# Performance work log

Measured on AMD Instinct MI355X. Metric: run time of the kernel, lower is better.

The kernel has to match this reference:

```python
import jax, jax.numpy as jnp
import numpy as np

D_MODEL = 1024
H = 16
D_K = D_MODEL // H
B, S = 4, 2048


def setup_inputs() -> dict:
    key = jax.random.key(0)
    ks = jax.random.split(key, 12)
    s = 1.0 / np.sqrt(D_MODEL)
    inp = {
        "q": jax.random.normal(ks[0], (B, S, D_MODEL), jnp.float32),
        "k": jax.random.normal(ks[1], (B, S, D_MODEL), jnp.float32),
        "v": jax.random.normal(ks[2], (B, S, D_MODEL), jnp.float32),
        "mask": jax.random.randint(ks[3], (1, 1, S, S), 0, 2, jnp.int32),
        # torch nn.Linear convention: weight [out, in], y = x @ W.T + b
        "w_q": jax.random.uniform(ks[4], (D_MODEL, D_MODEL), jnp.float32, -s, s),
        "b_q": jax.random.uniform(ks[5], (D_MODEL,), jnp.float32, -s, s),
        "w_k": jax.random.uniform(ks[6], (D_MODEL, D_MODEL), jnp.float32, -s, s),
        "b_k": jax.random.uniform(ks[7], (D_MODEL,), jnp.float32, -s, s),
        "w_v": jax.random.uniform(ks[8], (D_MODEL, D_MODEL), jnp.float32, -s, s),
        "b_v": jax.random.uniform(ks[9], (D_MODEL,), jnp.float32, -s, s),
        "w_o": jax.random.uniform(ks[10], (D_MODEL, D_MODEL), jnp.float32, -s, s),
        "b_o": jax.random.uniform(ks[11], (D_MODEL,), jnp.float32, -s, s),
    }
    return inp


def _split_heads(x):
    b, s, _ = x.shape
    return x.reshape(b, s, H, D_K).transpose(0, 2, 1, 3)  # [B,H,S,Dk]


def reference(q, k, v, mask, w_q, b_q, w_k, b_k, w_v, b_v, w_o, b_o):
    query = _split_heads(q @ w_q.T + b_q)
    key = _split_heads(k @ w_k.T + b_k)
    value = _split_heads(v @ w_v.T + b_v)
    scores = jnp.einsum("bhqd,bhkd->bhqk", query, key) / jnp.sqrt(
        jnp.asarray(D_K, query.dtype))
    scores = jnp.where(mask == 0, jnp.asarray(-1e9, scores.dtype), scores)
    attn = jax.nn.softmax(scores, axis=-1)  # dropout p=0 (eval) -> identity
    x = jnp.einsum("bhqk,bhkd->bhqd", attn, value)
    x = x.transpose(0, 2, 1, 3).reshape(q.shape[0], -1, H * D_K)
    return x @ w_o.T + b_o
```

## Files before the change

### kernel.cpp

```cpp
#include <hip/hip_runtime.h>

typedef __bf16 bf16_t;
typedef __bf16 bf16x4 __attribute__((ext_vector_type(4)));
typedef __bf16 bf16x8 __attribute__((ext_vector_type(8)));
typedef float f32x4 __attribute__((ext_vector_type(4)));
typedef float f32x16 __attribute__((ext_vector_type(16)));
typedef unsigned int uint;
typedef uint uint2v __attribute__((ext_vector_type(2)));
typedef uint uint4v __attribute__((ext_vector_type(4)));

#define CSCALE 0.18033688011112042f

static __device__ __forceinline__ bf16_t f2bf(float f) {
  unsigned u = __builtin_bit_cast(unsigned, f);
  u = (u + 0x7fff + ((u >> 16) & 1)) >> 16;
  unsigned short h = (unsigned short)u;
  return __builtin_bit_cast(bf16_t, h);
}
static __device__ __forceinline__ uint cvt_pk(float a, float b) {
  uint r;
  asm("v_cvt_pk_bf16_f32 %0, %1, %2" : "=v"(r) : "v"(a), "v"(b));
  return r;
}

#define GLD_LDS(g, l) \
  __builtin_amdgcn_global_load_lds((const __attribute__((address_space(1))) void*)(g), \
                                   (__attribute__((address_space(3))) void*)(l), 16, 0, 0)
#define VMCNT(n) asm volatile("s_waitcnt vmcnt(" #n ")" ::: "memory")
#define LGKM0() asm volatile("s_waitcnt lgkmcnt(0)" ::: "memory")
#define BARRIER() do { __builtin_amdgcn_s_barrier(); __builtin_amdgcn_sched_barrier(0); } while (0)

__global__ void cvt4_f2b(const float* __restrict__ a, const float* __restrict__ b,
                         const float* __restrict__ c, const float* __restrict__ d,
                         bf16_t* __restrict__ oa, bf16_t* __restrict__ ob,
                         bf16_t* __restrict__ oc, bf16_t* __restrict__ od) {
  int i = blockIdx.x * 256 + threadIdx.x;
  const float* src = a;
  bf16_t* dst = oa;
  int w = i >> 18;
  i &= 262143;
  if (w == 1) { src = b; dst = ob; }
  else if (w == 2) { src = c; dst = oc; }
  else if (w == 3) { src = d; dst = od; }
  const float4 f = reinterpret_cast<const float4*>(src)[i];
  bf16x4 o;
  o[0] = f2bf(f.x); o[1] = f2bf(f.y); o[2] = f2bf(f.z); o[3] = f2bf(f.w);
  reinterpret_cast<bf16x4*>(dst)[i] = o;
}

__global__ void mask_bits_k(const int* __restrict__ m, uint* __restrict__ out) {
  int i = blockIdx.x * 256 + threadIdx.x;
  int q = i & 2047, t = i >> 11;
  const int* mrow = m + (size_t)q * 2048 + t * 32;
  uint bits = 0;
#pragma unroll
  for (int j = 0; j < 16; ++j) {
    int r0 = (j & 3) + 8 * (j >> 2);
    bits |= (mrow[r0] ? 1u : 0u) << j;
    bits |= (mrow[r0 + 4] ? 1u : 0u) << (16 + j);
  }
  out[(size_t)t * 2048 + q] = bits;
}

__global__ __launch_bounds__(256, 2) void qkv_gemm(
    const float* __restrict__ qA, const float* __restrict__ kA, const float* __restrict__ vA,
    const bf16_t* __restrict__ wq, const bf16_t* __restrict__ wk, const bf16_t* __restrict__ wv,
    const float* __restrict__ bq, const float* __restrict__ bk, const float* __restrict__ bv,
    bf16_t* __restrict__ Qp, bf16_t* __restrict__ Kp, bf16_t* __restrict__ Vt) {
  constexpr int K = 1024;
  __shared__ __align__(16) bf16_t AsB[2][128 * 32];
  __shared__ __align__(16) bf16_t BsB[3][256 * 32];
  const int z = blockIdx.z;
  const float* A = (z == 0) ? qA : (z == 1) ? kA : vA;
  const bf16_t* W = (z == 0) ? wq : (z == 1) ? wk : wv;
  const float* bias = (z == 0) ? bq : (z == 1) ? bk : bv;

  const int tid = threadIdx.x;
  const int lane = tid & 63;
  const int wv_ = tid >> 6;
  const int wm = (wv_ & 1) * 64, wn = (wv_ >> 1) * 128;
  const int l15 = lane & 15, lhi = lane >> 4;
  const int bm = blockIdx.x, bn = blockIdx.y;

  const int arow0 = tid >> 3;
  const int acol = tid & 7;
  const float* gA = A + (size_t)(bm * 128 + arow0) * K + acol * 4;
  const int brows = tid >> 2;
  const bf16_t* gB = W + (size_t)(bn * 256 + brows) * K + ((tid & 3) ^ (brows & 3)) * 8;

  f32x4 acc[4][8] = {};
  f32x4 rA0[4], rA1[4];

  auto A_LOAD = [&](int t, f32x4* R) {
#pragma unroll
    for (int L = 0; L < 4; ++L)
      R[L] = *reinterpret_cast<const f32x4*>(gA + (size_t)L * 32 * K + t * 32);
  };
  auto A_WRITE = [&](const f32x4* R, int buf) {
#pragma unroll
    for (int L = 0; L < 4; ++L) {
      int row = arow0 + L * 32;
      uint2v u;
      u[0] = cvt_pk(R[L][0], R[L][1]);
      u[1] = cvt_pk(R[L][2], R[L][3]);
      char* p = (char*)&AsB[buf][0] + row * 64 + (((acol >> 1) ^ (row & 3)) * 16) + (acol & 1) * 8;
      *reinterpret_cast<uint2v*>(p) = u;
    }
  };
  auto B_STAGE = [&](int t, int buf) {
#pragma unroll
    for (int c2 = 0; c2 < 4; ++c2)
      GLD_LDS(gB + (size_t)c2 * 64 * K + t * 32, (char*)&BsB[buf][0] + c2 * 4096 + wv_ * 1024);
  };
  auto COMPUTE = [&](int ba, int bb) {
    bf16x8 af[4], bfv[8];
#pragma unroll
    for (int i = 0; i < 4; ++i) {
      int arow = wm + i * 16 + l15;
      af[i] = *reinterpret_cast<const bf16x8*>(
          (const char*)&AsB[ba][0] + arow * 64 + ((lhi ^ (arow & 3)) * 16));
    }
#pragma unroll
    for (int j = 0; j < 8; ++j) {
      int br = wn + j * 16 + l15;
      bfv[j] = *reinterpret_cast<const bf16x8*>(
          (const char*)&BsB[bb][0] + br * 64 + ((lhi ^ (br & 3)) * 16));
    }
#pragma unroll
    for (int i = 0; i < 4; ++i)
#pragma unroll
      for (int j = 0; j < 8; ++j)
        acc[i][j] = __builtin_amdgcn_mfma_f32_16x16x32_bf16(af[i], bfv[j], acc[i][j], 0, 0, 0);
  };

#define QSTEP(T, RL, RW, BAW, BAC, BBC, BBS) \
  A_LOAD((T) + 2, RL); B_STAGE((T) + 2, BBS); \
  COMPUTE(BAC, BBC); \
  VMCNT(8); \
  A_WRITE(RW, BAW); \
  LGKM0(); BARRIER();

  A_LOAD(0, rA0); B_STAGE(0, 0);
  A_LOAD(1, rA1); B_STAGE(1, 1);
  VMCNT(8);
  A_WRITE(rA0, 0);
  LGKM0(); BARRIER();

#pragma unroll 1
  for (int t6 = 0; t6 < 30; t6 += 6) {
    QSTEP(t6 + 0, rA0, rA1, 1, 0, 0, 2)
    QSTEP(t6 + 1, rA1, rA0, 0, 1, 1, 0)
    QSTEP(t6 + 2, rA0, rA1, 1, 0, 2, 1)
    QSTEP(t6 + 3, rA1, rA0, 0, 1, 0, 2)
    QSTEP(t6 + 4, rA0, rA1, 1, 0, 1, 0)
    QSTEP(t6 + 5, rA1, rA0, 0, 1, 2, 1)
  }
  COMPUTE(0, 0);
  VMCNT(4);
  A_WRITE(rA1, 1);
  VMCNT(0);
  LGKM0(); BARRIER();
  COMPUTE(1, 1);

  if (z == 2) {
    const int b = (bm * 128) >> 11;
    const int s0 = (bm * 128) & 2047;
    bf16_t* vb = Vt + ((size_t)b * 1024 + bn * 256 + wn + l15) * 2048 + s0 + wm + lhi * 4;
#pragma unroll
    for (int j = 0; j < 8; ++j) {
      float bv2 = bias[bn * 256 + wn + j * 16 + l15];
#pragma unroll
      for (int i = 0; i < 4; ++i) {
        bf16x4 pk;
#pragma unroll
        for (int r = 0; r < 4; ++r) pk[r] = f2bf(acc[i][j][r] + bv2);
        *reinterpret_cast<bf16x4*>(vb + (size_t)(j * 16) * 2048 + i * 16) = pk;
      }
    }
  } else {
    bf16_t* O = (z == 0) ? Qp : Kp;
    const float scale = (z == 0) ? CSCALE : 1.0f;
#pragma unroll
    for (int i = 0; i < 4; ++i) {
#pragma unroll
      for (int j = 0; j < 8; ++j) {
        int n = bn * 256 + wn + j * 16 + l15;
        float bv2 = bias[n];
#pragma unroll
        for (int r = 0; r < 4; ++r) {
          int m = bm * 128 + wm + i * 16 + lhi * 4 + r;
          O[(size_t)m * 1024 + n] = f2bf((acc[i][j][r] + bv2) * scale);
        }
      }
    }
  }
#undef QSTEP
}

__global__ __launch_bounds__(256, 2) void gemm_o(
    const bf16_t* __restrict__ A, const bf16_t* __restrict__ Bw,
    const float* __restrict__ bias, float* __restrict__ Cout) {
  constexpr int K = 1024;
  __shared__ __align__(16) bf16_t As[3][128 * 32];
  __shared__ __align__(16) bf16_t Bs[3][256 * 32];
  const int tid = threadIdx.x;
  const int lane = tid & 63;
  const int wv_ = tid >> 6;
  const int wm = (wv_ & 1) * 64, wn = (wv_ >> 1) * 128;
  const int l15 = lane & 15, lhi = lane >> 4;
  const int bm = blockIdx.x, bn = blockIdx.y;
  const int rws = tid >> 2;
  const bf16_t* ga = A + (size_t)(bm * 128 + rws) * K + ((tid & 3) ^ (rws & 3)) * 8;
  const bf16_t* gb = Bw + (size_t)(bn * 256 + rws) * K + ((tid & 3) ^ (rws & 3)) * 8;
  f32x4 acc[4][8] = {};

  auto STAGE = [&](int t, int buf) {
#pragma unroll
    for (int c2 = 0; c2 < 2; ++c2)
      GLD_LDS(ga + (size_t)c2 * 64 * K + t * 32, (char*)&As[buf][0] + c2 * 4096 + wv_ * 1024);
#pragma unroll
    for (int c2 = 0; c2 < 4; ++c2)
      GLD_LDS(gb + (size_t)c2 * 64 * K + t * 32, (char*)&Bs[buf][0] + c2 * 4096 + wv_ * 1024);
  };
  auto COMPUTE = [&](int buf) {
    bf16x8 af[4], bfv[8];
#pragma unroll
    for (int i = 0; i < 4; ++i) {
      int arow = wm + i * 16 + l15;
      af[i] = *reinterpret_cast<const bf16x8*>(
          (const char*)&As[buf][0] + arow * 64 + ((lhi ^ (arow & 3)) * 16));
    }
#pragma unroll
    for (int j = 0; j < 8; ++j) {
      int br = wn + j * 16 + l15;
      bfv[j] = *reinterpret_cast<const bf16x8*>(
          (const char*)&Bs[buf][0] + br * 64 + ((lhi ^ (br & 3)) * 16));
    }
#pragma unroll
    for (int i = 0; i < 4; ++i)
#pragma unroll
      for (int j = 0; j < 8; ++j)
        acc[i][j] = __builtin_amdgcn_mfma_f32_16x16x32_bf16(af[i], bfv[j], acc[i][j], 0, 0, 0);
  };

  STAGE(0, 0);
  STAGE(1, 1);
#pragma unroll 1
  for (int tt = 0; tt < 30; tt += 3) {
    VMCNT(6); BARRIER(); COMPUTE(0); STAGE(tt + 2, 2);
    VMCNT(6); BARRIER(); COMPUTE(1); STAGE(tt + 3, 0);
    VMCNT(6); BARRIER(); COMPUTE(2); STAGE(tt + 4, 1);
  }
  VMCNT(6); BARRIER(); COMPUTE(0);
  VMCNT(0); BARRIER(); COMPUTE(1);

#pragma unroll
  for (int i = 0; i < 4; ++i)
#pragma unroll
    for (int j = 0; j < 8; ++j) {
      int n = bn * 256 + wn + j * 16 + l15;
      float bv2 = bias[n];
#pragma unroll
      for (int r = 0; r < 4; ++r) {
        int m = bm * 128 + wm + i * 16 + lhi * 4 + r;
        Cout[(size_t)m * 1024 + n] = acc[i][j][r] + bv2;
      }
    }
}

static __device__ __forceinline__ void qk2(const bf16_t* Kbuf, const bf16x8 qfA[4],
                                           const bf16x8 qfB[4], int l31, int h,
                                           f32x16& sA, f32x16& sB) {
  sA = {}; sB = {};
  __builtin_amdgcn_s_setprio(1);
#pragma unroll
  for (int c = 0; c < 4; ++c) {
    bf16x8 kf = *reinterpret_cast<const bf16x8*>(Kbuf + l31 * 72 + h * 8 + 16 * c);
    sA = __builtin_amdgcn_mfma_f32_32x32x16_bf16(kf, qfA[c], sA, 0, 0, 0);
    sB = __builtin_amdgcn_mfma_f32_32x32x16_bf16(kf, qfB[c], sB, 0, 0, 0);
  }
  __builtin_amdgcn_s_setprio(0);
}

static __device__ __forceinline__ void softmax_tile(
    const f32x16& sv, uint mb, int h, f32x16& o0, f32x16& o1,
    float& mrun, float& lsum, bf16x8& pa0, bf16x8& pa1) {
  const uint mbh = mb >> (h << 4);
  float a0 = fmaxf(fmaxf(sv[0], sv[1]), sv[2]);
  float a1 = fmaxf(fmaxf(sv[3], sv[4]), sv[5]);
  float a2 = fmaxf(fmaxf(sv[6], sv[7]), sv[8]);
  float a3 = fmaxf(fmaxf(sv[9], sv[10]), sv[11]);
  float a4 = fmaxf(fmaxf(sv[12], sv[13]), sv[14]);
  float b0 = fmaxf(fmaxf(a0, a1), a2);
  float mt = fmaxf(fmaxf(b0, fmaxf(a3, a4)), sv[15]);
  if (!__all(mt - mrun <= 8.0f)) {
    float mtf = fmaxf(mt, __shfl_xor(mt, 32));
    float mnew = fmaxf(mrun, mtf);
    float alpha = __builtin_amdgcn_exp2f(mrun - mnew);
    lsum *= alpha;
#pragma unroll
    for (int r = 0; r < 16; ++r) {
      float ar = __shfl(alpha, (r & 3) + 8 * (r >> 2) + 4 * h);
      o0[r] *= ar; o1[r] *= ar;
    }
    mrun = mnew;
  }
  float p[16];
#pragma unroll
  for (int r = 0; r < 16; ++r) {
    float pv = __builtin_amdgcn_exp2f(sv[r] - mrun);
    uint smask = (uint)__builtin_amdgcn_sbfe((int)mbh, r, 1);
    p[r] = __builtin_bit_cast(float, __builtin_bit_cast(uint, pv) & smask);
  }
  float t0 = p[0] + p[1], t1 = p[2] + p[3], t2 = p[4] + p[5], t3 = p[6] + p[7];
  float t4 = p[8] + p[9], t5 = p[10] + p[11], t6 = p[12] + p[13], t7 = p[14] + p[15];
  t0 += t1; t2 += t3; t4 += t5; t6 += t7;
  lsum += (t0 + t2) + (t4 + t6);
  uint dw[8];
#pragma unroll
  for (int i = 0; i < 8; ++i) dw[i] = cvt_pk(p[2 * i], p[2 * i + 1]);
  uint e0 = (uint)__shfl_xor((int)(h ? dw[0] : dw[2]), 32);
  uint e1 = (uint)__shfl_xor((int)(h ? dw[1] : dw[3]), 32);
  uint e2 = (uint)__shfl_xor((int)(h ? dw[4] : dw[6]), 32);
  uint e3 = (uint)__shfl_xor((int)(h ? dw[5] : dw[7]), 32);
  uint4v ua0 = {h ? e0 : dw[0], h ? e1 : dw[1], h ? dw[2] : e0, h ? dw[3] : e1};
  uint4v ua1 = {h ? e2 : dw[4], h ? e3 : dw[5], h ? dw[6] : e2, h ? dw[7] : e3};
  pa0 = __builtin_bit_cast(bf16x8, ua0);
  pa1 = __builtin_bit_cast(bf16x8, ua1);
}

static __device__ __forceinline__ void pv2(const bf16_t* Vbuf,
                                           bf16x8 paA0, bf16x8 paA1, bf16x8 paB0, bf16x8 paB1,
                                           int l31, int h,
                                           f32x16& oA0, f32x16& oA1, f32x16& oB0, f32x16& oB1) {
  bf16x8 v00 = *reinterpret_cast<const bf16x8*>(Vbuf + l31 * 40 + h * 8);
  bf16x8 v01 = *reinterpret_cast<const bf16x8*>(Vbuf + l31 * 40 + 16 + h * 8);
  bf16x8 v10 = *reinterpret_cast<const bf16x8*>(Vbuf + (32 + l31) * 40 + h * 8);
  bf16x8 v11 = *reinterpret_cast<const bf16x8*>(Vbuf + (32 + l31) * 40 + 16 + h * 8);
  __builtin_amdgcn_s_setprio(1);
  oA0 = __builtin_amdgcn_mfma_f32_32x32x16_bf16(paA0, v00, oA0, 0, 0, 0);
  oA0 = __builtin_amdgcn_mfma_f32_32x32x16_bf16(paA1, v01, oA0, 0, 0, 0);
  oA1 = __builtin_amdgcn_mfma_f32_32x32x16_bf16(paA0, v10, oA1, 0, 0, 0);
  oA1 = __builtin_amdgcn_mfma_f32_32x32x16_bf16(paA1, v11, oA1, 0, 0, 0);
  oB0 = __builtin_amdgcn_mfma_f32_32x32x16_bf16(paB0, v00, oB0, 0, 0, 0);
  oB0 = __builtin_amdgcn_mfma_f32_32x32x16_bf16(paB1, v01, oB0, 0, 0, 0);
  oB1 = __builtin_amdgcn_mfma_f32_32x32x16_bf16(paB0, v10, oB1, 0, 0, 0);
  oB1 = __builtin_amdgcn_mfma_f32_32x32x16_bf16(paB1, v11, oB1, 0, 0, 0);
  __builtin_amdgcn_s_setprio(0);
}

__global__ __launch_bounds__(256, 2) void attn_kernel(
    const bf16_t* __restrict__ Qp, const bf16_t* __restrict__ Kp,
    const bf16_t* __restrict__ Vt, const uint* __restrict__ maskbits,
    bf16_t* __restrict__ Xb) {
  constexpr int S = 2048, D = 1024;
  __shared__ __align__(16) bf16_t Ks[2][32][72];
  __shared__ __align__(16) bf16_t Vs[2][64][40];
  const int tid = threadIdx.x;
  const int wv_ = tid >> 6, lane = tid & 63;
  const int l31 = lane & 31, h = lane >> 5;
  const int blk = blockIdx.x;
  const int bh = blk & 63, qt = blk >> 6;
  const int b = bh >> 4, hd = bh & 15;
  const int q0 = qt * 256 + wv_ * 64;

  const int rK = tid >> 3, sK = tid & 7;
  const int rV = tid >> 2, sV = tid & 3;
  const bf16_t* gK = Kp + ((size_t)b * S + rK) * D + hd * 64 + sK * 8;
  const bf16_t* gV = Vt + ((size_t)b * 1024 + hd * 64 + rV) * (size_t)S + sV * 8;
  bf16_t* wK0 = &Ks[0][rK][sK * 8];
  bf16_t* wK1 = &Ks[1][rK][sK * 8];
  bf16_t* wV0 = &Vs[0][rV][sV * 8];
  bf16_t* wV1 = &Vs[1][rV][sV * 8];

  const bf16_t* qbase = Qp + (size_t)(b * S + q0 + l31) * D + hd * 64 + h * 8;
  bf16x8 qfA[4], qfB[4];
#pragma unroll
  for (int c = 0; c < 4; ++c) {
    qfA[c] = *reinterpret_cast<const bf16x8*>(qbase + 16 * c);
    qfB[c] = *reinterpret_cast<const bf16x8*>(qbase + (size_t)32 * D + 16 * c);
  }

  const uint* mbase = maskbits + q0 + l31;

  f32x16 oA0 = {}, oA1 = {}, oB0 = {}, oB1 = {};
  float mrunA = 0.f, lsumA = 0.f, mrunB = 0.f, lsumB = 0.f;
  bf16x8 paA0, paA1, paB0, paB1;

  {
    bf16x8 k0 = *reinterpret_cast<const bf16x8*>(gK);
    bf16x8 k1 = *reinterpret_cast<const bf16x8*>(gK + (size_t)32 * D);
    bf16x8 v0 = *reinterpret_cast<const bf16x8*>(gV);
    *reinterpret_cast<bf16x8*>(wK0) = k0;
    *reinterpret_cast<bf16x8*>(wK1) = k1;
    *reinterpret_cast<bf16x8*>(wV0) = v0;
  }
  uint mbA = mbase[0], mbB = mbase[32];
  __syncthreads();
  {
    f32x16 sA, sB;
    qk2(&Ks[0][0][0], qfA, qfB, l31, h, sA, sB);
    softmax_tile(sA, mbA, h, oA0, oA1, mrunA, lsumA, paA0, paA1);
    softmax_tile(sB, mbB, h, oB0, oB1, mrunB, lsumB, paB0, paB1);
  }

  auto body = [&](int j, bf16_t* wK_st, bf16_t* wV_st, const bf16_t* Kq,
                  const bf16_t* Vp, bool stageK) {
    bf16x8 kreg, vreg;
    if (stageK) kreg = *reinterpret_cast<const bf16x8*>(gK + (size_t)(j + 2) * 32 * D);
    vreg = *reinterpret_cast<const bf16x8*>(gV + (size_t)(j + 1) * 32);
    uint mnA = mbase[(size_t)(j + 1) * 2048];
    uint mnB = mbase[(size_t)(j + 1) * 2048 + 32];
    f32x16 sA, sB;
    qk2(Kq, qfA, qfB, l31, h, sA, sB);
    pv2(Vp, paA0, paA1, paB0, paB1, l31, h, oA0, oA1, oB0, oB1);
    softmax_tile(sA, mnA, h, oA0, oA1, mrunA, lsumA, paA0, paA1);
    softmax_tile(sB, mnB, h, oB0, oB1, mrunB, lsumB, paB0, paB1);
    if (stageK) *reinterpret_cast<bf16x8*>(wK_st) = kreg;
    *reinterpret_cast<bf16x8*>(wV_st) = vreg;
    __syncthreads();
  };

#pragma unroll 1
  for (int jj = 0; jj < 31; ++jj) {
    const int j = 2 * jj;
    body(j,     wK0, wV1, &Ks[1][0][0], &Vs[0][0][0], true);
    body(j + 1, wK1, wV0, &Ks[0][0][0], &Vs[1][0][0], true);
  }
  body(62, wK0, wV1, &Ks[1][0][0], &Vs[0][0][0], false);
  pv2(&Vs[1][0][0], paA0, paA1, paB0, paB1, l31, h, oA0, oA1, oB0, oB1);

  lsumA += __shfl_xor(lsumA, 32);
  lsumB += __shfl_xor(lsumB, 32);
  float linvA = __builtin_amdgcn_rcpf(lsumA);
  float linvB = __builtin_amdgcn_rcpf(lsumB);
  bf16_t* xrow = Xb + (size_t)(b * S + q0) * D + hd * 64 + l31;
#pragma unroll
  for (int r = 0; r < 16; ++r) {
    int qrow = (r & 3) + 8 * (r >> 2) + 4 * h;
    float lrA = __shfl(linvA, qrow);
    float lrB = __shfl(linvB, qrow);
    xrow[(size_t)qrow * D] = f2bf(oA0[r] * lrA);
    xrow[(size_t)qrow * D + 32] = f2bf(oA1[r] * lrA);
    xrow[(size_t)(qrow + 32) * D] = f2bf(oB0[r] * lrB);
    xrow[(size_t)(qrow + 32) * D + 32] = f2bf(oB1[r] * lrB);
  }
}

extern "C" void kernel_launch(void* const* d_in, const int* in_sizes, int n_in,
                              void* d_out, int out_size, void* d_ws, size_t ws_size,
                              hipStream_t stream) {
  const float* q = (const float*)d_in[0];
  const float* k = (const float*)d_in[1];
  const float* v = (const float*)d_in[2];
  const int* mask = (const int*)d_in[3];
  const float* w_q = (const float*)d_in[4];
  const float* b_q = (const float*)d_in[5];
  const float* w_k = (const float*)d_in[6];
  const float* b_k = (const float*)d_in[7];
  const float* w_v = (const float*)d_in[8];
  const float* b_v = (const float*)d_in[9];
  const float* w_o = (const float*)d_in[10];
  const float* b_o = (const float*)d_in[11];

  char* ws = (char*)d_ws;
  const size_t SZ = (size_t)8192 * 1024 * 2;
  bf16_t* Qp = (bf16_t*)(ws + 0 * SZ);
  bf16_t* Kp = (bf16_t*)(ws + 1 * SZ);
  bf16_t* Vt = (bf16_t*)(ws + 2 * SZ);
  bf16_t* Xb = (bf16_t*)(ws + 3 * SZ);
  uint* maskB = (uint*)(ws + 4 * SZ);
  bf16_t* wqb = (bf16_t*)(ws + 4 * SZ + 8388608);
  bf16_t* wkb = wqb + 1048576;
  bf16_t* wvb = wkb + 1048576;
  bf16_t* wob = wvb + 1048576;

  cvt4_f2b<<<4096, 256, 0, stream>>>(w_q, w_k, w_v, w_o, wqb, wkb, wvb, wob);
  mask_bits_k<<<512, 256, 0, stream>>>(mask, maskB);

  dim3 g3(64, 4, 3);
  qkv_gemm<<<g3, 256, 0, stream>>>(q, k, v, wqb, wkb, wvb, b_q, b_k, b_v, Qp, Kp, Vt);
  attn_kernel<<<512, 256, 0, stream>>>(Qp, Kp, Vt, maskB, Xb);
  gemm_o<<<dim3(64, 4), 256, 0, stream>>>(Xb, wob, b_o, (float*)d_out);
}
```

Measured before the change: 235.1 us.

## Give each wave private K/V LDS buffers and remove block-wide barriers

Each of the four waves now loads its own copy of the K and V tiles into a private double-buffered LDS region, so the per-tile __syncthreads is removed. The software pipeline is also simplified: the deferred PV-after-QK skew is dropped, and the next tile's global loads are prefetched into registers while the current tile is computed. The cost is four times the global/L2 traffic for K/V and four times the LDS footprint, which may reduce occupancy. With no barrier, correctness depends on wave-level ordering of LDS writes and reads within a single wave.

```diff
diff --git a/kernel.cpp b/kernel.cpp
--- a/kernel.cpp
+++ b/kernel.cpp
@@ -354,8 +354,8 @@
     const bf16_t* __restrict__ Vt, const uint* __restrict__ maskbits,
     bf16_t* __restrict__ Xb) {
   constexpr int S = 2048, D = 1024;
-  __shared__ __align__(16) bf16_t Ks[2][32][72];
-  __shared__ __align__(16) bf16_t Vs[2][64][40];
+  __shared__ __align__(16) bf16_t Ks[4][2][32][72];
+  __shared__ __align__(16) bf16_t Vs[4][2][64][40];
   const int tid = threadIdx.x;
   const int wv_ = tid >> 6, lane = tid & 63;
   const int l31 = lane & 31, h = lane >> 5;
@@ -364,14 +364,10 @@
   const int b = bh >> 4, hd = bh & 15;
   const int q0 = qt * 256 + wv_ * 64;
 
-  const int rK = tid >> 3, sK = tid & 7;
-  const int rV = tid >> 2, sV = tid & 3;
-  const bf16_t* gK = Kp + ((size_t)b * S + rK) * D + hd * 64 + sK * 8;
-  const bf16_t* gV = Vt + ((size_t)b * 1024 + hd * 64 + rV) * (size_t)S + sV * 8;
-  bf16_t* wK0 = &Ks[0][rK][sK * 8];
-  bf16_t* wK1 = &Ks[1][rK][sK * 8];
-  bf16_t* wV0 = &Vs[0][rV][sV * 8];
-  bf16_t* wV1 = &Vs[1][rV][sV * 8];
+  const int kRow = lane >> 3, kSlot = lane & 7;
+  const int vRow = lane >> 2, vSlot = lane & 3;
+  const bf16_t* gK = Kp + ((size_t)b * S + kRow) * D + hd * 64 + kSlot * 8;
+  const bf16_t* gV = Vt + ((size_t)b * 1024 + hd * 64 + vRow) * (size_t)S + vSlot * 8;
 
   const bf16_t* qbase = Qp + (size_t)(b * S + q0 + l31) * D + hd * 64 + h * 8;
   bf16x8 qfA[4], qfB[4];
@@ -387,48 +383,56 @@
   float mrunA = 0.f, lsumA = 0.f, mrunB = 0.f, lsumB = 0.f;
   bf16x8 paA0, paA1, paB0, paB1;
 
+  auto K_LOAD = [&](int t, bf16x8* R) {
+#pragma unroll
+    for (int c = 0; c < 4; ++c)
+      R[c] = *reinterpret_cast<const bf16x8*>(gK + (size_t)(t * 32 + 8 * c) * D);
+  };
+  auto V_LOAD = [&](int t, bf16x8* R) {
+#pragma unroll
+    for (int c = 0; c < 4; ++c)
+      R[c] = *reinterpret_cast<const bf16x8*>(gV + (size_t)(16 * c) * S + t * 32);
+  };
+  auto K_WRITE = [&](const bf16x8* R, int buf) {
+#pragma unroll
+    for (int c = 0; c < 4; ++c)
+      *reinterpret_cast<bf16x8*>(&Ks[wv_][buf][8 * c + kRow][kSlot * 8]) = R[c];
+  };
+  auto V_WRITE = [&](const bf16x8* R, int buf) {
+#pragma unroll
+    for (int c = 0; c < 4; ++c)
+      *reinterpret_cast<bf16x8*>(&Vs[wv_][buf][16 * c + vRow][vSlot * 8]) = R[c];
+  };
+
   {
-    bf16x8 k0 = *reinterpret_cast<const bf16x8*>(gK);
-    bf16x8 k1 = *reinterpret_cast<const bf16x8*>(gK + (size_t)32 * D);
-    bf16x8 v0 = *reinterpret_cast<const bf16x8*>(gV);
-    *reinterpret_cast<bf16x8*>(wK0) = k0;
-    *reinterpret_cast<bf16x8*>(wK1) = k1;
-    *reinterpret_cast<bf16x8*>(wV0) = v0;
-  }
-  uint mbA = mbase[0], mbB = mbase[32];
-  __syncthreads();
-  {
+    bf16x8 kr[4], vr[4];
+    K_LOAD(0, kr);
+    V_LOAD(0, vr);
+    K_WRITE(kr, 0);
+    V_WRITE(vr, 0);
+  }
+
+#pragma unroll 2
+  for (int t = 0; t < 64; ++t) {
+    const int cur = t & 1, nxt = cur ^ 1;
+    const bool pf = (t < 63);
+    bf16x8 kr[4], vr[4];
+    if (pf) {
+      K_LOAD(t + 1, kr);
+      V_LOAD(t + 1, vr);
+    }
+    uint mnA = mbase[(size_t)t * 2048];
+    uint mnB = mbase[(size_t)t * 2048 + 32];
     f32x16 sA, sB;
-    qk2(&Ks[0][0][0], qfA, qfB, l31, h, sA, sB);
-    softmax_tile(sA, mbA, h, oA0, oA1, mrunA, lsumA, paA0, paA1);
-    softmax_tile(sB, mbB, h, oB0, oB1, mrunB, lsumB, paB0, paB1);
-  }
-
-  auto body = [&](int j, bf16_t* wK_st, bf16_t* wV_st, const bf16_t* Kq,
-                  const bf16_t* Vp, bool stageK) {
-    bf16x8 kreg, vreg;
-    if (stageK) kreg = *reinterpret_cast<const bf16x8*>(gK + (size_t)(j + 2) * 32 * D);
-    vreg = *reinterpret_cast<const bf16x8*>(gV + (size_t)(j + 1) * 32);
-    uint mnA = mbase[(size_t)(j + 1) * 2048];
-    uint mnB = mbase[(size_t)(j + 1) * 2048 + 32];
-    f32x16 sA, sB;
-    qk2(Kq, qfA, qfB, l31, h, sA, sB);
-    pv2(Vp, paA0, paA1, paB0, paB1, l31, h, oA0, oA1, oB0, oB1);
+    qk2(&Ks[wv_][cur][0][0], qfA, qfB, l31, h, sA, sB);
     softmax_tile(sA, mnA, h, oA0, oA1, mrunA, lsumA, paA0, paA1);
     softmax_tile(sB, mnB, h, oB0, oB1, mrunB, lsumB, paB0, paB1);
-    if (stageK) *reinterpret_cast<bf16x8*>(wK_st) = kreg;
-    *reinterpret_cast<bf16x8*>(wV_st) = vreg;
-    __syncthreads();
-  };
-
-#pragma unroll 1
-  for (int jj = 0; jj < 31; ++jj) {
-    const int j = 2 * jj;
-    body(j,     wK0, wV1, &Ks[1][0][0], &Vs[0][0][0], true);
-    body(j + 1, wK1, wV0, &Ks[0][0][0], &Vs[1][0][0], true);
-  }
-  body(62, wK0, wV1, &Ks[1][0][0], &Vs[0][0][0], false);
-  pv2(&Vs[1][0][0], paA0, paA1, paB0, paB1, l31, h, oA0, oA1, oB0, oB1);
+    pv2(&Vs[wv_][cur][0][0], paA0, paA1, paB0, paB1, l31, h, oA0, oA1, oB0, oB1);
+    if (pf) {
+      K_WRITE(kr, nxt);
+      V_WRITE(vr, nxt);
+    }
+  }
 
   lsumA += __shfl_xor(lsumA, 32);
   lsumB += __shfl_xor(lsumB, 32);
```

Result: faster. 226.1 us (median of 2 runs) (-3.8%).
